# Performance work log

Measured on AMD Instinct MI355X. Metric: run time of the kernel, lower is better.

The kernel has to match this reference:

```python
import jax, jax.numpy as jnp
import numpy as np

B = 384          # batch; must equal F for the final broadcast to be valid
F = 384          # out_features
H = 64           # hidden_dim
TAU = 1.0        # d_k passed to attention()
EPS = 1e-12      # F.normalize eps


def _l2_normalize(x):
    # torch F.normalize(p=2, dim=-1): x / max(||x||, eps)
    n = jnp.sqrt(jnp.sum(x * x, axis=-1, keepdims=True))
    return x / jnp.maximum(n, EPS)


def setup_inputs() -> dict:
    key = jax.random.key(0)
    kx, kwq, kbq, kwk, kbk = jax.random.split(key, 5)
    bound = 1.0 / np.sqrt(F)  # torch Linear default init range
    x = jax.random.normal(kx, (B, F), dtype=jnp.float32)
    Wq = jax.random.uniform(kwq, (F * H, F), jnp.float32, -bound, bound)
    bq = jax.random.uniform(kbq, (F * H,), jnp.float32, -bound, bound)
    Wk = jax.random.uniform(kwk, (F * H, F), jnp.float32, -bound, bound)
    bk = jax.random.uniform(kbk, (F * H,), jnp.float32, -bound, bound)
    return {"x": x, "Wq": Wq, "bq": bq, "Wk": Wk, "bk": bk}


def reference(x, Wq, bq, Wk, bk):
    # q = qs(x), k = ks(x): [B, F*H] -> reshape [B, F, H]
    q = (x @ Wq.T + bq).reshape(B, F, H)
    k = (x @ Wk.T + bk).reshape(B, F, H)
    # L2-normalized QK attention with temperature sqrt(tau)
    q = _l2_normalize(q)
    k = _l2_normalize(k)
    scores = jnp.einsum('bfh,bgh->bfg', q, k) / jnp.sqrt(jnp.float32(TAU))
    scores = jax.nn.softmax(scores, axis=-1)  # [B, F, F]
    # faithful to `input * scores`: x[B,F] left-pads to [1,B,F]; valid since B==F
    return x * scores
```

## Files before the change

### kernel.cpp

```cpp
#include <hip/hip_runtime.h>
#include <hip/hip_bf16.h>


typedef __attribute__((ext_vector_type(8))) short bf16x8;
typedef __attribute__((ext_vector_type(4))) float f32x4;

__device__ __forceinline__ ushort f2bf(float f) {
  union { __hip_bfloat16 h; ushort u; } c;
  c.h = __float2bfloat16(f);
  return c.u;
}

__device__ __forceinline__ void load_lds16(const void* g, void* l) {
  __builtin_amdgcn_global_load_lds(
      (const __attribute__((address_space(1))) void*)g,
      (__attribute__((address_space(3))) void*)l, 16, 0, 0);
}

__global__ __launch_bounds__(256) void xconv(const float* __restrict__ xin,
                                             ushort* __restrict__ xbf) {
  int t = blockIdx.x * 256 + threadIdx.x;
  int o = t * 8;
  int kt = o / 12288;
  int rem = o - kt * 12288;
  int m = rem >> 5;
  int sp = (rem >> 3) & 3;
  int slot = sp ^ ((m >> 1) & 3);
  const float* src = xin + m * 384 + kt * 32 + slot * 8;
  float4 a = *reinterpret_cast<const float4*>(src);
  float4 b = *reinterpret_cast<const float4*>(src + 4);
  ushort4 u0 = make_ushort4(f2bf(a.x), f2bf(a.y), f2bf(a.z), f2bf(a.w));
  ushort4 u1 = make_ushort4(f2bf(b.x), f2bf(b.y), f2bf(b.z), f2bf(b.w));
  *reinterpret_cast<ushort4*>(xbf + o)     = u0;
  *reinterpret_cast<ushort4*>(xbf + o + 4) = u1;
}

__global__ __launch_bounds__(256) void qk_gemm(
    const ushort* __restrict__ xbf,
    const float* __restrict__ Wq, const float* __restrict__ bq,
    const float* __restrict__ Wk, const float* __restrict__ bk,
    ushort* __restrict__ qhat, ushort* __restrict__ khat)
{
  const int bx = blockIdx.x;
  const int n0 = bx * 64;
  const float* W    = blockIdx.y ? Wk : Wq;
  const float* bias = blockIdx.y ? bk : bq;
  ushort* outp      = blockIdx.y ? khat : qhat;

  __shared__ __align__(16) ushort Alds[384 * 32];
  __shared__ __align__(16) ushort Blds[64 * 40];

  const int tid  = threadIdx.x;
  const int wave = tid >> 6;
  const int lane = tid & 63;
  const int l15  = lane & 15;
  const int lhi  = lane >> 4;

  f32x4 acc[6][4];
  #pragma unroll
  for (int m = 0; m < 6; ++m)
    #pragma unroll
    for (int n = 0; n < 4; ++n) acc[m][n] = (f32x4)(0.f);

  const int aslot = lhi ^ ((l15 >> 1) & 3);

  for (int kt = 0; kt < 12; ++kt) {
    const ushort* asrc = xbf + kt * 12288 + lane * 8;
    #pragma unroll
    for (int i = 0; i < 6; ++i) {
      int chunk = wave * 6 + i;
      load_lds16(asrc + chunk * 512, (char*)Alds + chunk * 1024);
    }
    #pragma unroll
    for (int i = 0; i < 2; ++i) {
      int idx = tid + 256 * i;
      int row = idx >> 3, c4 = idx & 7;
      float4 v = *reinterpret_cast<const float4*>(
          W + (size_t)(n0 + row) * 384 + kt * 32 + c4 * 4);
      ushort4 u = make_ushort4(f2bf(v.x), f2bf(v.y), f2bf(v.z), f2bf(v.w));
      *reinterpret_cast<ushort4*>(&Blds[row * 40 + c4 * 4]) = u;
    }
    __syncthreads();

    bf16x8 bfr[4];
    #pragma unroll
    for (int nf = 0; nf < 4; ++nf)
      bfr[nf] = *reinterpret_cast<const bf16x8*>(&Blds[(nf * 16 + l15) * 40 + lhi * 8]);
    #pragma unroll
    for (int mf = 0; mf < 6; ++mf) {
      int rr = wave * 96 + mf * 16 + l15;
      bf16x8 afr = *reinterpret_cast<const bf16x8*>(&Alds[rr * 32 + aslot * 8]);
      #pragma unroll
      for (int nf = 0; nf < 4; ++nf)
        acc[mf][nf] = __builtin_amdgcn_mfma_f32_16x16x32_bf16(afr, bfr[nf], acc[mf][nf], 0, 0, 0);
    }
    __syncthreads();
  }

  float bv[4];
  #pragma unroll
  for (int nf = 0; nf < 4; ++nf) bv[nf] = bias[n0 + nf * 16 + l15];

  float scl[6][4];
  #pragma unroll
  for (int mf = 0; mf < 6; ++mf) {
    float ss[4];
    #pragma unroll
    for (int j = 0; j < 4; ++j) {
      float s = 0.f;
      #pragma unroll
      for (int nf = 0; nf < 4; ++nf) {
        float v = acc[mf][nf][j] + bv[nf];
        acc[mf][nf][j] = v;
        s += v * v;
      }
      ss[j] = s;
    }
    #pragma unroll
    for (int m = 1; m < 16; m <<= 1) {
      #pragma unroll
      for (int j = 0; j < 4; ++j) ss[j] += __shfl_xor(ss[j], m, 64);
    }
    #pragma unroll
    for (int j = 0; j < 4; ++j)
      scl[mf][j] = 1.f / fmaxf(sqrtf(ss[j]), 1e-12f);
  }

  const int sw = bx & 7;
  ushort* E = Alds + wave * 3072;
  #pragma unroll
  for (int hh = 0; hh < 2; ++hh) {
    __syncthreads();
    #pragma unroll
    for (int lmf = 0; lmf < 3; ++lmf) {
      const int mf = hh * 3 + lmf;
      #pragma unroll
      for (int nf = 0; nf < 4; ++nf)
        #pragma unroll
        for (int j = 0; j < 4; ++j)
          E[(lmf * 16 + lhi * 4 + j) * 64 + nf * 16 + l15] =
              f2bf(acc[mf][nf][j] * scl[mf][j]);
    }
    __syncthreads();
    #pragma unroll
    for (int i = 0; i < 6; ++i) {
      int lr = i * 8 + (lane >> 3);
      int q  = lane & 7;
      bf16x8 v = *reinterpret_cast<const bf16x8*>(&E[lr * 64 + ((q ^ sw) << 3)]);
      int grow = wave * 96 + hh * 48 + lr;
      *reinterpret_cast<bf16x8*>(outp + (size_t)grow * 24576 + n0 + q * 8) = v;
    }
  }
}

#define PSTR 392
__global__ __launch_bounds__(256, 3) void attn_out(
    const float* __restrict__ xin,
    const ushort* __restrict__ qhat,
    const ushort* __restrict__ khat,
    float* __restrict__ out)
{
  const int id  = blockIdx.x;
  const int xcd = id & 7;
  const int j_  = id >> 3;
  const int b   = xcd * 48 + j_ / 6;
  const int f0  = (j_ % 6) * 64;

  __shared__ __align__(16) char smem[32 * PSTR * 4];
  ushort* Klds = reinterpret_cast<ushort*>(smem);
  float*  Slds = reinterpret_cast<float*>(smem);

  const int tid  = threadIdx.x;
  const int wave = tid >> 6;
  const int lane = tid & 63;
  const int l15  = lane & 15;
  const int lhi  = lane >> 4;

  const ushort* ksrc = khat + (size_t)b * 24576 + lane * 8;
  #pragma unroll
  for (int i = 0; i < 12; ++i) {
    int chunk = wave * 12 + i;
    load_lds16(ksrc + chunk * 512, (char*)Klds + chunk * 1024);
  }

  const int fr = f0 + wave * 16 + l15;
  bf16x8 q8[2];
  #pragma unroll
  for (int ks = 0; ks < 2; ++ks)
    q8[ks] = *reinterpret_cast<const bf16x8*>(
        qhat + (size_t)b * 24576 + (size_t)fr * 64 + (((ks * 4 + lhi) ^ (l15 & 7)) << 3));
  __syncthreads();

  f32x4 acc[24];
  #pragma unroll
  for (int n = 0; n < 24; ++n) acc[n] = (f32x4)(0.f);

  #pragma unroll
  for (int ks = 0; ks < 2; ++ks) {
    #pragma unroll
    for (int nf = 0; nf < 24; ++nf) {
      bf16x8 kf = *reinterpret_cast<const bf16x8*>(
          &Klds[(nf * 16 + l15) * 64 + (((ks * 4 + lhi) ^ (l15 & 7)) << 3)]);
      acc[nf] = __builtin_amdgcn_mfma_f32_16x16x32_bf16(kf, q8[ks], acc[nf], 0, 0, 0);
    }
  }

  float m0 = acc[0][0], m1 = acc[0][1], m2 = acc[0][2], m3 = acc[0][3];
  #pragma unroll
  for (int nf = 1; nf < 24; ++nf) {
    m0 = fmaxf(m0, acc[nf][0]); m1 = fmaxf(m1, acc[nf][1]);
    m2 = fmaxf(m2, acc[nf][2]); m3 = fmaxf(m3, acc[nf][3]);
  }
  float m = fmaxf(fmaxf(m0, m1), fmaxf(m2, m3));
  m = fmaxf(m, __shfl_xor(m, 16, 64));
  m = fmaxf(m, __shfl_xor(m, 32, 64));

  float s0 = 0.f, s1 = 0.f, s2 = 0.f, s3 = 0.f;
  #pragma unroll
  for (int nf = 0; nf < 24; ++nf) {
    float p0 = __expf(acc[nf][0] - m);
    float p1 = __expf(acc[nf][1] - m);
    float p2 = __expf(acc[nf][2] - m);
    float p3 = __expf(acc[nf][3] - m);
    acc[nf][0] = p0; acc[nf][1] = p1; acc[nf][2] = p2; acc[nf][3] = p3;
    s0 += p0; s1 += p1; s2 += p2; s3 += p3;
  }
  float s = (s0 + s1) + (s2 + s3);
  s += __shfl_xor(s, 16, 64);
  s += __shfl_xor(s, 32, 64);
  const float inv = 1.f / s;

  __syncthreads();

  #pragma unroll
  for (int half = 0; half < 2; ++half) {
    if ((wave >> 1) == half) {
      const int prow = (wave & 1) * 16 + l15;
      #pragma unroll
      for (int nf = 0; nf < 24; ++nf) {
        f32x4 v;
        v[0] = acc[nf][0] * inv; v[1] = acc[nf][1] * inv;
        v[2] = acc[nf][2] * inv; v[3] = acc[nf][3] * inv;
        *reinterpret_cast<f32x4*>(&Slds[prow * PSTR + nf * 16 + lhi * 4]) = v;
      }
    }
    __syncthreads();

    const int rbase = f0 + half * 32;
    const float* xsrc = xin + (size_t)rbase * 384;
    float* odst = out + (size_t)b * 147456 + (size_t)rbase * 384;
    #pragma unroll
    for (int i = 0; i < 12; ++i) {
      int idx = tid + 256 * i;
      int row = idx / 96, c = idx - row * 96;
      float4 p4 = *reinterpret_cast<const float4*>(&Slds[row * PSTR + c * 4]);
      float4 x4 = *reinterpret_cast<const float4*>(xsrc + row * 384 + c * 4);
      float4 o;
      o.x = x4.x * p4.x;  o.y = x4.y * p4.y;
      o.z = x4.z * p4.z;  o.w = x4.w * p4.w;
      *reinterpret_cast<float4*>(odst + row * 384 + c * 4) = o;
    }
    if (half == 0) __syncthreads();
  }
}

extern "C" void kernel_launch(void* const* d_in, const int* in_sizes, int n_in,
                              void* d_out, int out_size, void* d_ws, size_t ws_size,
                              hipStream_t stream) {
  const float* x  = (const float*)d_in[0];
  const float* Wq = (const float*)d_in[1];
  const float* bq = (const float*)d_in[2];
  const float* Wk = (const float*)d_in[3];
  const float* bk = (const float*)d_in[4];
  float* out = (float*)d_out;

  ushort* qhat = (ushort*)d_ws;
  ushort* khat = qhat + (size_t)384 * 24576;
  ushort* xbf  = khat + (size_t)384 * 24576;

  xconv<<<dim3(72), dim3(256), 0, stream>>>(x, xbf);

  dim3 g1(384, 2), b1(256);
  qk_gemm<<<g1, b1, 0, stream>>>(xbf, Wq, bq, Wk, bk, qhat, khat);

  attn_out<<<dim3(2304), dim3(256), 0, stream>>>(x, qhat, khat, out);
}
```

Before: 114.3 us.

## Double-buffer weight tiles with register prefetch and split K-tile loads in attention

The projection GEMM now double-buffers the bf16 weight tile in LDS and prefetches fp32 weights two k-steps ahead in registers. Manual waitcnt and barriers replace the paired __syncthreads, so global loads overlap the MFMA work. The attention kernel interleaves the K-tile chunk assignment across waves and waits on only the first half before starting MFMAs on it, hiding the rest of the load. A launch-bounds occupancy hint of 3 is also added. The risks are more register pressure and fragile hand-written vmcnt counting.

```diff
diff --git a/kernel.cpp b/kernel.cpp
--- a/kernel.cpp
+++ b/kernel.cpp
@@ -35,7 +35,7 @@
   *reinterpret_cast<ushort4*>(xbf + o + 4) = u1;
 }
 
-__global__ __launch_bounds__(256) void qk_gemm(
+__global__ __launch_bounds__(256, 3) void qk_gemm(
     const ushort* __restrict__ xbf,
     const float* __restrict__ Wq, const float* __restrict__ bq,
     const float* __restrict__ Wk, const float* __restrict__ bk,
@@ -48,7 +48,7 @@
   ushort* outp      = blockIdx.y ? khat : qhat;
 
   __shared__ __align__(16) ushort Alds[384 * 32];
-  __shared__ __align__(16) ushort Blds[64 * 40];
+  __shared__ __align__(16) ushort Blds[2][64 * 40];
 
   const int tid  = threadIdx.x;
   const int wave = tid >> 6;
@@ -56,6 +56,9 @@
   const int l15  = lane & 15;
   const int lhi  = lane >> 4;
 
+  const int wrow = tid >> 3;
+  const int wc4  = (tid & 7) * 4;
+
   f32x4 acc[6][4];
   #pragma unroll
   for (int m = 0; m < 6; ++m)
@@ -64,38 +67,78 @@
 
   const int aslot = lhi ^ ((l15 >> 1) & 3);
 
-  for (int kt = 0; kt < 12; ++kt) {
-    const ushort* asrc = xbf + kt * 12288 + lane * 8;
-    #pragma unroll
-    for (int i = 0; i < 6; ++i) {
-      int chunk = wave * 6 + i;
-      load_lds16(asrc + chunk * 512, (char*)Alds + chunk * 1024);
-    }
-    #pragma unroll
-    for (int i = 0; i < 2; ++i) {
-      int idx = tid + 256 * i;
-      int row = idx >> 3, c4 = idx & 7;
-      float4 v = *reinterpret_cast<const float4*>(
-          W + (size_t)(n0 + row) * 384 + kt * 32 + c4 * 4);
-      ushort4 u = make_ushort4(f2bf(v.x), f2bf(v.y), f2bf(v.z), f2bf(v.w));
-      *reinterpret_cast<ushort4*>(&Blds[row * 40 + c4 * 4]) = u;
-    }
-    __syncthreads();
-
-    bf16x8 bfr[4];
-    #pragma unroll
-    for (int nf = 0; nf < 4; ++nf)
-      bfr[nf] = *reinterpret_cast<const bf16x8*>(&Blds[(nf * 16 + l15) * 40 + lhi * 8]);
-    #pragma unroll
-    for (int mf = 0; mf < 6; ++mf) {
-      int rr = wave * 96 + mf * 16 + l15;
-      bf16x8 afr = *reinterpret_cast<const bf16x8*>(&Alds[rr * 32 + aslot * 8]);
-      #pragma unroll
-      for (int nf = 0; nf < 4; ++nf)
-        acc[mf][nf] = __builtin_amdgcn_mfma_f32_16x16x32_bf16(afr, bfr[nf], acc[mf][nf], 0, 0, 0);
-    }
-    __syncthreads();
-  }
+  float4 sXa, sXb, sYa, sYb;
+  {
+    const float* w0 = W + (size_t)(n0 + wrow) * 384 + wc4;
+    sXa = *reinterpret_cast<const float4*>(w0);
+    sXb = *reinterpret_cast<const float4*>(w0 + 32 * 384);
+    sYa = *reinterpret_cast<const float4*>(w0 + 32);
+    sYb = *reinterpret_cast<const float4*>(w0 + 32 * 384 + 32);
+  }
+  {
+    ushort4 u0 = make_ushort4(f2bf(sXa.x), f2bf(sXa.y), f2bf(sXa.z), f2bf(sXa.w));
+    ushort4 u1 = make_ushort4(f2bf(sXb.x), f2bf(sXb.y), f2bf(sXb.z), f2bf(sXb.w));
+    *reinterpret_cast<ushort4*>(&Blds[0][wrow * 40 + wc4])        = u0;
+    *reinterpret_cast<ushort4*>(&Blds[0][(wrow + 32) * 40 + wc4]) = u1;
+    const float* w2 = W + (size_t)(n0 + wrow) * 384 + 2 * 32 + wc4;
+    sXa = *reinterpret_cast<const float4*>(w2);
+    sXb = *reinterpret_cast<const float4*>(w2 + 32 * 384);
+  }
+  asm volatile("s_waitcnt lgkmcnt(0)" ::: "memory");
+  __builtin_amdgcn_s_barrier();
+  __builtin_amdgcn_sched_barrier(0);
+
+#define GEMM_STEP(kt, Wa, Wb)                                                  \
+  {                                                                            \
+                   \
+    ushort* Bn = Blds[((kt) + 1) & 1];                                         \
+    ushort4 u0 = make_ushort4(f2bf(Wa.x), f2bf(Wa.y), f2bf(Wa.z), f2bf(Wa.w)); \
+    ushort4 u1 = make_ushort4(f2bf(Wb.x), f2bf(Wb.y), f2bf(Wb.z), f2bf(Wb.w)); \
+    *reinterpret_cast<ushort4*>(&Bn[wrow * 40 + wc4])        = u0;             \
+    *reinterpret_cast<ushort4*>(&Bn[(wrow + 32) * 40 + wc4]) = u1;             \
+                               \
+    const ushort* asrc = xbf + (kt) * 12288 + lane * 8;                        \
+    _Pragma("unroll")                                                          \
+    for (int i = 0; i < 6; ++i) {                                              \
+      int chunk = wave * 6 + i;                                                \
+      load_lds16(asrc + chunk * 512, (char*)Alds + chunk * 1024);              \
+    }                                                                          \
+                              \
+    {                                                                          \
+      int ktp = (kt) + 3 <= 11 ? (kt) + 3 : 11;                                \
+      const float* wp = W + (size_t)(n0 + wrow) * 384 + ktp * 32 + wc4;        \
+      Wa = *reinterpret_cast<const float4*>(wp);                               \
+      Wb = *reinterpret_cast<const float4*>(wp + 32 * 384);                    \
+    }                                                                          \
+                     \
+    asm volatile("s_waitcnt vmcnt(2)" ::: "memory");                           \
+    __builtin_amdgcn_sched_barrier(0);                                         \
+    const ushort* Bc = Blds[(kt) & 1];                                         \
+    bf16x8 bfr[4];                                                             \
+    _Pragma("unroll")                                                          \
+    for (int nf = 0; nf < 4; ++nf)                                             \
+      bfr[nf] = *reinterpret_cast<const bf16x8*>(                              \
+          &Bc[(nf * 16 + l15) * 40 + lhi * 8]);                                \
+    _Pragma("unroll")                                                          \
+    for (int mf = 0; mf < 6; ++mf) {                                           \
+      int rr = wave * 96 + mf * 16 + l15;                                      \
+      bf16x8 afr = *reinterpret_cast<const bf16x8*>(&Alds[rr * 32 + aslot * 8]); \
+      _Pragma("unroll")                                                        \
+      for (int nf = 0; nf < 4; ++nf)                                           \
+        acc[mf][nf] = __builtin_amdgcn_mfma_f32_16x16x32_bf16(                 \
+            afr, bfr[nf], acc[mf][nf], 0, 0, 0);                               \
+    }                                                                          \
+       \
+    asm volatile("s_waitcnt lgkmcnt(0)" ::: "memory");                         \
+    __builtin_amdgcn_s_barrier();                                              \
+    __builtin_amdgcn_sched_barrier(0);                                         \
+  }
+
+  for (int kt2 = 0; kt2 < 12; kt2 += 2) {
+    GEMM_STEP(kt2,     sYa, sYb)
+    GEMM_STEP(kt2 + 1, sXa, sXb)
+  }
+#undef GEMM_STEP
 
   float bv[4];
   #pragma unroll
@@ -176,29 +219,50 @@
   const int l15  = lane & 15;
   const int lhi  = lane >> 4;
 
-  const ushort* ksrc = khat + (size_t)b * 24576 + lane * 8;
-  #pragma unroll
-  for (int i = 0; i < 12; ++i) {
-    int chunk = wave * 12 + i;
-    load_lds16(ksrc + chunk * 512, (char*)Klds + chunk * 1024);
-  }
-
   const int fr = f0 + wave * 16 + l15;
   bf16x8 q8[2];
   #pragma unroll
   for (int ks = 0; ks < 2; ++ks)
     q8[ks] = *reinterpret_cast<const bf16x8*>(
         qhat + (size_t)b * 24576 + (size_t)fr * 64 + (((ks * 4 + lhi) ^ (l15 & 7)) << 3));
-  __syncthreads();
+  __builtin_amdgcn_sched_barrier(0);
+
+  const ushort* ksrc = khat + (size_t)b * 24576 + lane * 8;
+  #pragma unroll
+  for (int i = 0; i < 6; ++i) {
+    int chunk = wave + 4 * i;
+    load_lds16(ksrc + chunk * 512, (char*)Klds + chunk * 1024);
+  }
+  __builtin_amdgcn_sched_barrier(0);
+  #pragma unroll
+  for (int i = 6; i < 12; ++i) {
+    int chunk = wave + 4 * i;
+    load_lds16(ksrc + chunk * 512, (char*)Klds + chunk * 1024);
+  }
 
   f32x4 acc[24];
   #pragma unroll
   for (int n = 0; n < 24; ++n) acc[n] = (f32x4)(0.f);
 
+  asm volatile("s_waitcnt vmcnt(6)" ::: "memory");
+  __builtin_amdgcn_s_barrier();
+  __builtin_amdgcn_sched_barrier(0);
   #pragma unroll
   for (int ks = 0; ks < 2; ++ks) {
     #pragma unroll
-    for (int nf = 0; nf < 24; ++nf) {
+    for (int nf = 0; nf < 12; ++nf) {
+      bf16x8 kf = *reinterpret_cast<const bf16x8*>(
+          &Klds[(nf * 16 + l15) * 64 + (((ks * 4 + lhi) ^ (l15 & 7)) << 3)]);
+      acc[nf] = __builtin_amdgcn_mfma_f32_16x16x32_bf16(kf, q8[ks], acc[nf], 0, 0, 0);
+    }
+  }
+  asm volatile("s_waitcnt vmcnt(0)" ::: "memory");
+  __builtin_amdgcn_s_barrier();
+  __builtin_amdgcn_sched_barrier(0);
+  #pragma unroll
+  for (int ks = 0; ks < 2; ++ks) {
+    #pragma unroll
+    for (int nf = 12; nf < 24; ++nf) {
       bf16x8 kf = *reinterpret_cast<const bf16x8*>(
           &Klds[(nf * 16 + l15) * 64 + (((ks * 4 + lhi) ^ (l15 & 7)) << 3)]);
       acc[nf] = __builtin_amdgcn_mfma_f32_16x16x32_bf16(kf, q8[ks], acc[nf], 0, 0, 0);
```

Result: slower. 140.3 us (+22.7%).
